# Performance work log

Measured on AMD Instinct MI355X. Metric: run time of the kernel, lower is better.

## Reference

```python
import jax, jax.numpy as jnp
import numpy as np
from jax import lax

K = 7            # pool_size / PSROI_BINS
C_OUT = 10       # output channels per bin (features has K*K*C_OUT channels)
FEAT_STRIDE = 16
LAMDA = 0.1
SAMPLES = 2      # bilinear sample points per bin side
H = W = 200
C_IN = K * K * C_OUT  # 490
N_ROIS = 512


def setup_inputs() -> dict:
    key = jax.random.key(0)
    k1, k2, k3, k4 = jax.random.split(key, 4)
    features = jax.random.normal(k1, (1, H, W, C_IN), jnp.float32)
    conv_w = jax.random.truncated_normal(k2, -2.0, 2.0, (3, 3, C_IN, 2 * K * K), jnp.float32) * 0.01
    img = H * FEAT_STRIDE  # image-space extent
    cxy = jax.random.uniform(k3, (N_ROIS, 2), minval=0.0, maxval=img - 1.0)
    wh = jax.random.uniform(k4, (N_ROIS, 2), minval=64.0, maxval=640.0)
    x1 = jnp.clip(cxy[:, 0] - wh[:, 0] * 0.5, 0.0, img - 2.0)
    y1 = jnp.clip(cxy[:, 1] - wh[:, 1] * 0.5, 0.0, img - 2.0)
    x2 = jnp.clip(x1 + wh[:, 0], x1 + 1.0, img - 1.0)
    y2 = jnp.clip(y1 + wh[:, 1], y1 + 1.0, img - 1.0)
    rois = jnp.stack([jnp.zeros(N_ROIS), x1, y1, x2, y2], axis=-1)  # [N,5]
    return {"features": features, "rois": rois, "conv_w": conv_w}


def _bilinear(feat, y, x):
    """feat [H,W,C]; y,x arbitrary equal shapes -> [..., C]."""
    Hf, Wf = feat.shape[0], feat.shape[1]
    y = jnp.clip(y, 0.0, Hf - 1.0)
    x = jnp.clip(x, 0.0, Wf - 1.0)
    y0 = jnp.floor(y)
    x0 = jnp.floor(x)
    y0i = y0.astype(jnp.int32)
    x0i = x0.astype(jnp.int32)
    y1i = jnp.minimum(y0i + 1, Hf - 1)
    x1i = jnp.minimum(x0i + 1, Wf - 1)
    wy = (y - y0)[..., None]
    wx = (x - x0)[..., None]
    v00 = feat[y0i, x0i]
    v01 = feat[y0i, x1i]
    v10 = feat[y1i, x0i]
    v11 = feat[y1i, x1i]
    return (v00 * (1 - wy) * (1 - wx) + v01 * (1 - wy) * wx
            + v10 * wy * (1 - wx) + v11 * wy * wx)


def _ps_roi(feat, box, cpg, offsets):
    """Position-sensitive RoI avg pooling with optional per-bin offsets.
    feat [H,W,K*K*cpg]; box (x1,y1,x2,y2) image coords; offsets [K,K,2] (dx,dy)
    in image coords or None. Returns [K,K,cpg]."""
    x1, y1, x2, y2 = box
    fx1 = x1 / FEAT_STRIDE
    fy1 = y1 / FEAT_STRIDE
    bw = (x2 - x1 + 1.0) / FEAT_STRIDE / K
    bh = (y2 - y1 + 1.0) / FEAT_STRIDE / K
    idx = jnp.arange(K, dtype=feat.dtype)
    s = (jnp.arange(SAMPLES, dtype=feat.dtype) + 0.5) / SAMPLES
    sx = fx1 + (idx[:, None] + s[None, :]) * bw  # [K(j), S]
    sy = fy1 + (idx[:, None] + s[None, :]) * bh  # [K(i), S]
    gx = jnp.broadcast_to(sx[None, :, None, :], (K, K, SAMPLES, SAMPLES))
    gy = jnp.broadcast_to(sy[:, None, :, None], (K, K, SAMPLES, SAMPLES))
    if offsets is not None:
        off = offsets / FEAT_STRIDE  # image -> feature coords
        gx = gx + off[..., 0][:, :, None, None]
        gy = gy + off[..., 1][:, :, None, None]
    vals = _bilinear(feat, gy, gx)                     # [K,K,S,S,K*K*cpg]
    vals = vals.reshape(K, K, SAMPLES, SAMPLES, K * K, cpg)
    bin_idx = (jnp.arange(K)[:, None] * K + jnp.arange(K)[None, :])  # [K,K]
    sel = jnp.take_along_axis(
        vals, bin_idx[:, :, None, None, None, None], axis=4)[..., 0, :]
    return sel.mean(axis=(2, 3))  # [K,K,cpg]


def reference(features, rois, conv_w):
    # 3x3 same conv producing 2*K*K offset channels (no bias)
    offset_map = lax.conv_general_dilated(
        features, conv_w, (1, 1), 'SAME',
        dimension_numbers=('NHWC', 'HWIO', 'NHWC'))[0]  # [H,W,2*K*K]
    feat0 = features[0]  # [H,W,K*K*C_OUT]

    def one_roi(roi):
        x1, y1, x2, y2 = roi[1], roi[2], roi[3], roi[4]
        rw = x2 - x1 + 1.0
        rh = y2 - y1 + 1.0
        box = (x1, y1, x2, y2)
        # stage 1: pool the offset map position-sensitively -> [K,K,2]
        off = _ps_roi(offset_map, box, 2, None).reshape(-1, 2)
        off = jnp.stack((off[:, 0] * rw * LAMDA,
                         off[:, 1] * rh * LAMDA), axis=-1).reshape(K, K, 2)
        # stage 2: deformable PS-RoI pooling of the features -> [K,K,C_OUT]
        return _ps_roi(feat0, box, C_OUT, off)

    return jax.vmap(one_roi)(rois)  # [N, K, K, C_OUT]
```

## Files before the change

### kernel.cpp

```cpp
#include <hip/hip_runtime.h>
#include <hip/hip_bf16.h>

#define Hh   200
#define Ww   200
#define CIN  490
#define OCN  98
#define KK   7
#define COUT 10
#define NROIS 512
#define PIX  8

#define PH   202
#define PW   202
#define PC   512
#define NPIX (Hh * Ww)
#define KCN  16
#define NF   7
#define NUNITS 144
#define NGRAN  36

typedef __attribute__((ext_vector_type(8))) short short8;
typedef __attribute__((ext_vector_type(4))) float float4v;

__global__ __launch_bounds__(256) void pack_feat_kernel(
    const float* __restrict__ feat, __hip_bfloat16* __restrict__ pf)
{
    int tid = blockIdx.x * 256 + threadIdx.x;
    if (tid >= PH * PW * (PC / 8)) return;
    int c8  = (tid & 63) * 8;
    int pix = tid >> 6;
    int py = pix / PW, px = pix % PW;
    __hip_bfloat16* dst = pf + (size_t)pix * PC + c8;
    bool interior = (py >= 1 && py <= Hh && px >= 1 && px <= Ww);

    __hip_bfloat16 v[8];
    if (interior && c8 + 8 <= CIN) {
        const float* s = feat + ((size_t)(py - 1) * Ww + (px - 1)) * CIN + c8;
#pragma unroll
        for (int q = 0; q < 4; ++q) {
            float2 f2 = *reinterpret_cast<const float2*>(s + q * 2);
            v[q * 2]     = __float2bfloat16(f2.x);
            v[q * 2 + 1] = __float2bfloat16(f2.y);
        }
    } else {
        const float* s = interior ? feat + ((size_t)(py - 1) * Ww + (px - 1)) * CIN : nullptr;
#pragma unroll
        for (int j = 0; j < 8; ++j) {
            float val = (interior && (c8 + j) < CIN) ? s[c8 + j] : 0.f;
            v[j] = __float2bfloat16(val);
        }
    }
    *reinterpret_cast<short8*>(dst) = *reinterpret_cast<short8*>(v);
}

__global__ __launch_bounds__(256) void pack_w_kernel(
    const float* __restrict__ w, __hip_bfloat16* __restrict__ bp)
{
    int idx = blockIdx.x * 256 + threadIdx.x;
    if (idx >= NUNITS * NF * 64 * 8) return;
    int j = idx & 7;
    int l = (idx >> 3) & 63;
    int f = (idx >> 9) % NF;
    int u = idx / (NF * 512);
    int tap = u / KCN, kc = u % KCN;
    int k = kc * 32 + ((l >> 4) * 8) + j;
    int n = f * 16 + (l & 15);
    float val = (k < CIN && n < OCN) ? w[((size_t)tap * CIN + k) * OCN + n] : 0.f;
    bp[idx] = __float2bfloat16(val);
}

__global__ __launch_bounds__(640) void conv_mfma_kernel(
    const short* __restrict__ pf,
    const short* __restrict__ bp,
    float* __restrict__ om)
{
    __shared__ short bsm[8 * 3584];

    int l = threadIdx.x & 63;
    int w = threadIdx.x >> 6;
    int m0 = blockIdx.x * 160 + w * 16;

    int row = m0 + (l & 15);
    int y = row / Ww, x = row % Ww;
    const short* abase = pf + ((size_t)(y * PW + x) * PC) + ((l >> 4) * 8);

    float4v acc[NF];
#pragma unroll
    for (int f = 0; f < NF; ++f) acc[f] = (float4v){0.f, 0.f, 0.f, 0.f};

    auto aAddr = [&](int u) -> const short* {
        int tap = u >> 4, kc = u & 15;
        int ky = tap / 3, kx = tap % 3;
        return abase + (ky * PW + kx) * PC + kc * 32;
    };

    {
#pragma unroll
        for (int s = 0; s < 3; ++s) {
            int i = w + s * 10;
            if (i < 28) {
                int u = i / 7, f = i % 7;
                short8 v = *reinterpret_cast<const short8*>(
                    bp + ((size_t)(u * NF + f)) * 512 + l * 8);
                *reinterpret_cast<short8*>(&bsm[(u & 7) * 3584 + f * 512 + l * 8]) = v;
            }
        }
    }
    short8 a0 = *reinterpret_cast<const short8*>(aAddr(0));
    short8 a1 = *reinterpret_cast<const short8*>(aAddr(1));
    short8 a2 = *reinterpret_cast<const short8*>(aAddr(2));
    short8 a3 = *reinterpret_cast<const short8*>(aAddr(3));
    __syncthreads();

    for (int g = 0; g < NGRAN; ++g) {
        bool more = (g < NGRAN - 1);
        int u0n = (g + 1) * 4;

        short8 st0, st1, st2;
        int off0 = -1, off1 = -1, off2 = -1;
        if (more) {
            {
                int i = w;
                int uu = u0n + i / 7, f = i % 7;
                st0 = *reinterpret_cast<const short8*>(
                    bp + ((size_t)(uu * NF + f)) * 512 + l * 8);
                off0 = (uu & 7) * 3584 + f * 512 + l * 8;
            }
            {
                int i = w + 10;
                int uu = u0n + i / 7, f = i % 7;
                st1 = *reinterpret_cast<const short8*>(
                    bp + ((size_t)(uu * NF + f)) * 512 + l * 8);
                off1 = (uu & 7) * 3584 + f * 512 + l * 8;
            }
            if (w + 20 < 28) {
                int i = w + 20;
                int uu = u0n + i / 7, f = i % 7;
                st2 = *reinterpret_cast<const short8*>(
                    bp + ((size_t)(uu * NF + f)) * 512 + l * 8);
                off2 = (uu & 7) * 3584 + f * 512 + l * 8;
            }
        }
        short8 n0, n1, n2, n3;
        if (more) {
            n0 = *reinterpret_cast<const short8*>(aAddr(u0n + 0));
            n1 = *reinterpret_cast<const short8*>(aAddr(u0n + 1));
            n2 = *reinterpret_cast<const short8*>(aAddr(u0n + 2));
            n3 = *reinterpret_cast<const short8*>(aAddr(u0n + 3));
        }

        int u0 = g * 4;
#define COMPUTE_UNIT(J, AREG)                                                   \
        {                                                                       \
            int sbase = ((u0 + J) & 7) * 3584 + l * 8;                          \
            _Pragma("unroll")                                                   \
            for (int f = 0; f < NF; ++f) {                                      \
                short8 b = *reinterpret_cast<short8*>(&bsm[sbase + f * 512]);   \
                acc[f] = __builtin_amdgcn_mfma_f32_16x16x32_bf16(               \
                    AREG, b, acc[f], 0, 0, 0);                                  \
            }                                                                   \
        }
        COMPUTE_UNIT(0, a0)
        COMPUTE_UNIT(1, a1)
        COMPUTE_UNIT(2, a2)
        COMPUTE_UNIT(3, a3)
#undef COMPUTE_UNIT

        if (off0 >= 0) *reinterpret_cast<short8*>(&bsm[off0]) = st0;
        if (off1 >= 0) *reinterpret_cast<short8*>(&bsm[off1]) = st1;
        if (off2 >= 0) *reinterpret_cast<short8*>(&bsm[off2]) = st2;
        if (more) { a0 = n0; a1 = n1; a2 = n2; a3 = n3; }
        __syncthreads();
    }

    int n = l & 15;
    int rbase = m0 + ((l >> 4) * 4);
#pragma unroll
    for (int f = 0; f < NF; ++f) {
        int col = f * 16 + n;
        if (col < OCN) {
#pragma unroll
            for (int j = 0; j < 4; ++j)
                om[(size_t)(rbase + j) * OCN + col] = acc[f][j];
        }
    }
}

__global__ __launch_bounds__(256) void conv3x3_kernel(
    const float* __restrict__ feat, const float* __restrict__ w,
    const float* __restrict__ zero, float* __restrict__ om)
{
    int idx = blockIdx.x * blockDim.x + threadIdx.x;
    if (idx >= Hh * (Ww / PIX) * OCN) return;
    int oc = idx % OCN;
    int g  = idx / OCN;
    int x0 = (g % (Ww / PIX)) * PIX;
    int y  = g / (Ww / PIX);

    float acc[PIX];
#pragma unroll
    for (int p = 0; p < PIX; ++p) acc[p] = 0.f;

    for (int ky = 0; ky < 3; ++ky) {
        int yy = y + ky - 1;
        if (yy < 0 || yy >= Hh) continue;
        const float* frow = feat + (size_t)yy * Ww * CIN;
        for (int kx = 0; kx < 3; ++kx) {
            const float* wp = w + ((ky * 3 + kx) * CIN) * OCN + oc;
            const float* fp[PIX];
#pragma unroll
            for (int p = 0; p < PIX; ++p) {
                int xx = x0 + p + kx - 1;
                fp[p] = (xx >= 0 && xx < Ww) ? (frow + (size_t)xx * CIN) : zero;
            }
            for (int ic = 0; ic < CIN; ic += 2) {
                float w0 = wp[ic * OCN];
                float w1 = wp[(ic + 1) * OCN];
#pragma unroll
                for (int p = 0; p < PIX; ++p) {
                    float2 f = *reinterpret_cast<const float2*>(fp[p] + ic);
                    acc[p] = fmaf(f.x, w0, acc[p]);
                    acc[p] = fmaf(f.y, w1, acc[p]);
                }
            }
        }
    }
    float* orow = om + ((size_t)y * Ww + x0) * OCN + oc;
#pragma unroll
    for (int p = 0; p < PIX; ++p) orow[p * OCN] = acc[p];
}

__device__ __forceinline__ void bilin_setup(float y, float x,
    int& i00, int& i01, int& i10, int& i11,
    float& w00, float& w01, float& w10, float& w11)
{
    y = fminf(fmaxf(y, 0.f), 199.f);
    x = fminf(fmaxf(x, 0.f), 199.f);
    float y0f = floorf(y), x0f = floorf(x);
    int y0 = (int)y0f, x0i = (int)x0f;
    int y1 = min(y0 + 1, 199), x1 = min(x0i + 1, 199);
    float wy = y - y0f, wx = x - x0f;
    i00 = y0 * Ww + x0i;  i01 = y0 * Ww + x1;
    i10 = y1 * Ww + x0i;  i11 = y1 * Ww + x1;
    w00 = (1.f - wy) * (1.f - wx);
    w01 = (1.f - wy) * wx;
    w10 = wy * (1.f - wx);
    w11 = wy * wx;
}

__global__ __launch_bounds__(256) void psroi_kernel(
    const float* __restrict__ feat, const float* __restrict__ rois,
    const float* __restrict__ om, float* __restrict__ out)
{
    int n = blockIdx.x;
    int t = threadIdx.x;

    float x1 = rois[n * 5 + 1], y1 = rois[n * 5 + 2];
    float x2 = rois[n * 5 + 3], y2 = rois[n * 5 + 4];
    float rw = x2 - x1 + 1.0f, rh = y2 - y1 + 1.0f;
    float fx1 = x1 * 0.0625f, fy1 = y1 * 0.0625f;
    float bw = (rw * 0.0625f) / 7.0f;
    float bh = (rh * 0.0625f) / 7.0f;

    __shared__ float offs[49][2];

    if (t < 49) {
        int bi = t / 7, bj = t % 7;
        float ax = 0.f, ay = 0.f;
#pragma unroll
        for (int ss = 0; ss < 4; ++ss) {
            float sj = ((float)(ss & 1) + 0.5f) * 0.5f;
            float si = ((float)(ss >> 1) + 0.5f) * 0.5f;
            float gx = fx1 + ((float)bj + sj) * bw;
            float gy = fy1 + ((float)bi + si) * bh;
            int i00, i01, i10, i11; float w00, w01, w10, w11;
            bilin_setup(gy, gx, i00, i01, i10, i11, w00, w01, w10, w11);
            int c0 = t * 2;
            const float* p00 = om + (size_t)i00 * OCN + c0;
            const float* p01 = om + (size_t)i01 * OCN + c0;
            const float* p10 = om + (size_t)i10 * OCN + c0;
            const float* p11 = om + (size_t)i11 * OCN + c0;
            ax += w00 * p00[0] + w01 * p01[0] + w10 * p10[0] + w11 * p11[0];
            ay += w00 * p00[1] + w01 * p01[1] + w10 * p10[1] + w11 * p11[1];
        }
        offs[t][0] = ax * 0.25f * rw * 0.1f * 0.0625f;
        offs[t][1] = ay * 0.25f * rh * 0.1f * 0.0625f;
    }
    __syncthreads();

    for (int o = t; o < KK * KK * COUT; o += blockDim.x) {
        int bin = o / COUT, c = o % COUT;
        int bi = bin / 7, bj = bin % 7;
        float dx = offs[bin][0], dy = offs[bin][1];
        int ch = bin * COUT + c;
        float acc = 0.f;
#pragma unroll
        for (int ss = 0; ss < 4; ++ss) {
            float sj = ((float)(ss & 1) + 0.5f) * 0.5f;
            float si = ((float)(ss >> 1) + 0.5f) * 0.5f;
            float gx = fx1 + ((float)bj + sj) * bw + dx;
            float gy = fy1 + ((float)bi + si) * bh + dy;
            int i00, i01, i10, i11; float w00, w01, w10, w11;
            bilin_setup(gy, gx, i00, i01, i10, i11, w00, w01, w10, w11);
            acc += w00 * feat[(size_t)i00 * CIN + ch]
                 + w01 * feat[(size_t)i01 * CIN + ch]
                 + w10 * feat[(size_t)i10 * CIN + ch]
                 + w11 * feat[(size_t)i11 * CIN + ch];
        }
        out[(size_t)n * (KK * KK * COUT) + o] = acc * 0.25f;
    }
}

extern "C" void kernel_launch(void* const* d_in, const int* in_sizes, int n_in,
                              void* d_out, int out_size, void* d_ws, size_t ws_size,
                              hipStream_t stream) {
    const float* feat = (const float*)d_in[0];
    const float* rois = (const float*)d_in[1];
    const float* w    = (const float*)d_in[2];
    float* out = (float*)d_out;

    const size_t OM_BYTES = (size_t)NPIX * OCN * 4;
    const size_t BP_BYTES = (size_t)NUNITS * NF * 64 * 8 * 2;
    const size_t PF_BYTES = (size_t)PH * PW * PC * 2;
    const size_t NEEDED = OM_BYTES + BP_BYTES + PF_BYTES;

    if (ws_size >= NEEDED) {
        float* om = (float*)d_ws;
        __hip_bfloat16* bp = (__hip_bfloat16*)((char*)d_ws + OM_BYTES);
        __hip_bfloat16* pf = (__hip_bfloat16*)((char*)d_ws + OM_BYTES + BP_BYTES);

        int wThreads = NUNITS * NF * 64 * 8;
        pack_w_kernel<<<(wThreads + 255) / 256, 256, 0, stream>>>(w, bp);
        int fThreads = PH * PW * (PC / 8);
        pack_feat_kernel<<<(fThreads + 255) / 256, 256, 0, stream>>>(feat, pf);
        conv_mfma_kernel<<<250, 640, 0, stream>>>(
            (const short*)pf, (const short*)bp, om);
        psroi_kernel<<<NROIS, 256, 0, stream>>>(feat, rois, om, out);
    } else {
        float* zero = (float*)d_ws;
        float* om   = (float*)d_ws + 1024;
        hipMemsetAsync(d_ws, 0, 4096, stream);
        int convThreads = Hh * (Ww / PIX) * OCN;
        conv3x3_kernel<<<(convThreads + 255) / 256, 256, 0, stream>>>(feat, w, zero, om);
        psroi_kernel<<<NROIS, 256, 0, stream>>>(feat, rois, om, out);
    }
}
```

Baseline: 96.75 us.

## Fuse feature bf16 packing into conv MFMA kernel and vectorize psroi gather

Removes the separate pack_feat kernel that converted and padded the features to bf16, and makes the conv MFMA kernel read the fp32 features directly. Padding is handled with per-tap boundary masks, and the tail of the channel range with a guarded partial load. The reduction order changes to kc-major/tap-minor, with pack_w updated to match, and the conv kernel gets a two-blocks-per-SM launch bound. The psroi stage-2 loop now has each thread handle two channels with float2 loads and stores. This saves a full write and reread of the padded bf16 feature buffer and one launch, but the conv loads double in bytes and need in-loop conversion and branching.

```diff
diff --git a/kernel.cpp b/kernel.cpp
--- a/kernel.cpp
+++ b/kernel.cpp
@@ -10,9 +10,6 @@
 #define NROIS 512
 #define PIX  8
 
-#define PH   202
-#define PW   202
-#define PC   512
 #define NPIX (Hh * Ww)
 #define KCN  16
 #define NF   7
@@ -21,37 +18,6 @@
 
 typedef __attribute__((ext_vector_type(8))) short short8;
 typedef __attribute__((ext_vector_type(4))) float float4v;
-
-__global__ __launch_bounds__(256) void pack_feat_kernel(
-    const float* __restrict__ feat, __hip_bfloat16* __restrict__ pf)
-{
-    int tid = blockIdx.x * 256 + threadIdx.x;
-    if (tid >= PH * PW * (PC / 8)) return;
-    int c8  = (tid & 63) * 8;
-    int pix = tid >> 6;
-    int py = pix / PW, px = pix % PW;
-    __hip_bfloat16* dst = pf + (size_t)pix * PC + c8;
-    bool interior = (py >= 1 && py <= Hh && px >= 1 && px <= Ww);
-
-    __hip_bfloat16 v[8];
-    if (interior && c8 + 8 <= CIN) {
-        const float* s = feat + ((size_t)(py - 1) * Ww + (px - 1)) * CIN + c8;
-#pragma unroll
-        for (int q = 0; q < 4; ++q) {
-            float2 f2 = *reinterpret_cast<const float2*>(s + q * 2);
-            v[q * 2]     = __float2bfloat16(f2.x);
-            v[q * 2 + 1] = __float2bfloat16(f2.y);
-        }
-    } else {
-        const float* s = interior ? feat + ((size_t)(py - 1) * Ww + (px - 1)) * CIN : nullptr;
-#pragma unroll
-        for (int j = 0; j < 8; ++j) {
-            float val = (interior && (c8 + j) < CIN) ? s[c8 + j] : 0.f;
-            v[j] = __float2bfloat16(val);
-        }
-    }
-    *reinterpret_cast<short8*>(dst) = *reinterpret_cast<short8*>(v);
-}
 
 __global__ __launch_bounds__(256) void pack_w_kernel(
     const float* __restrict__ w, __hip_bfloat16* __restrict__ bp)
@@ -62,15 +28,15 @@
     int l = (idx >> 3) & 63;
     int f = (idx >> 9) % NF;
     int u = idx / (NF * 512);
-    int tap = u / KCN, kc = u % KCN;
+    int kc = u / 9, tap = u % 9;
     int k = kc * 32 + ((l >> 4) * 8) + j;
     int n = f * 16 + (l & 15);
     float val = (k < CIN && n < OCN) ? w[((size_t)tap * CIN + k) * OCN + n] : 0.f;
     bp[idx] = __float2bfloat16(val);
 }
 
-__global__ __launch_bounds__(640) void conv_mfma_kernel(
-    const short* __restrict__ pf,
+__global__ __launch_bounds__(640, 2) void conv_mfma_kernel(
+    const float* __restrict__ feat,
     const short* __restrict__ bp,
     float* __restrict__ om)
 {
@@ -82,39 +48,91 @@
 
     int row = m0 + (l & 15);
     int y = row / Ww, x = row % Ww;
-    const short* abase = pf + ((size_t)(y * PW + x) * PC) + ((l >> 4) * 8);
+    int grp4 = l >> 4;
+    int grpOff = grp4 * 8;
+    int pixBase = (y * Ww + x) * CIN;
+
+    int smask = 0;
+#pragma unroll
+    for (int tp = 0; tp < 9; ++tp) {
+        int yy = y + tp / 3 - 1, xx = x + tp % 3 - 1;
+        if (yy >= 0 && yy < Hh && xx >= 0 && xx < Ww) smask |= (1 << tp);
+    }
 
     float4v acc[NF];
 #pragma unroll
     for (int f = 0; f < NF; ++f) acc[f] = (float4v){0.f, 0.f, 0.f, 0.f};
 
-    auto aAddr = [&](int u) -> const short* {
-        int tap = u >> 4, kc = u & 15;
-        int ky = tap / 3, kx = tap % 3;
-        return abase + (ky * PW + kx) * PC + kc * 32;
-    };
-
-    {
-#pragma unroll
-        for (int s = 0; s < 3; ++s) {
-            int i = w + s * 10;
-            if (i < 28) {
-                int u = i / 7, f = i % 7;
-                short8 v = *reinterpret_cast<const short8*>(
-                    bp + ((size_t)(u * NF + f)) * 512 + l * 8);
-                *reinterpret_cast<short8*>(&bsm[(u & 7) * 3584 + f * 512 + l * 8]) = v;
-            }
-        }
-    }
-    short8 a0 = *reinterpret_cast<const short8*>(aAddr(0));
-    short8 a1 = *reinterpret_cast<const short8*>(aAddr(1));
-    short8 a2 = *reinterpret_cast<const short8*>(aAddr(2));
-    short8 a3 = *reinterpret_cast<const short8*>(aAddr(3));
+    float2 preq[4][4];
+    short8 c0, c1, c2, c3;
+
+#define LOAD_A(J, UEXPR)                                                        \
+    {                                                                           \
+        int u_ = (UEXPR);                                                       \
+        int kc_ = u_ / 9, tap_ = u_ - kc_ * 9;                                  \
+        int toff_ = ((tap_ / 3 - 1) * Ww + (tap_ % 3 - 1)) * CIN;               \
+        bool v_ = (smask >> tap_) & 1;                                          \
+        const float* p_ = feat + (pixBase + toff_ + kc_ * 32 + grpOff);         \
+        float2 z_ = {0.f, 0.f};                                                 \
+        preq[J][0] = z_; preq[J][1] = z_; preq[J][2] = z_; preq[J][3] = z_;     \
+        if (kc_ < 15) {                                                         \
+            if (v_) {                                                           \
+                preq[J][0] = *reinterpret_cast<const float2*>(p_);              \
+                preq[J][1] = *reinterpret_cast<const float2*>(p_ + 2);          \
+                preq[J][2] = *reinterpret_cast<const float2*>(p_ + 4);          \
+                preq[J][3] = *reinterpret_cast<const float2*>(p_ + 6);          \
+            }                                                                   \
+        } else {                                                                \
+            if (v_ && grp4 == 0) {                                              \
+                preq[J][0] = *reinterpret_cast<const float2*>(p_);              \
+                preq[J][1] = *reinterpret_cast<const float2*>(p_ + 2);          \
+                preq[J][2] = *reinterpret_cast<const float2*>(p_ + 4);          \
+                preq[J][3] = *reinterpret_cast<const float2*>(p_ + 6);          \
+            } else if (v_ && grp4 == 1) {                                       \
+                preq[J][0] = *reinterpret_cast<const float2*>(p_);   \
+            }                                                                   \
+        }                                                                       \
+    }
+
+#define CVT_A(J, DST)                                                           \
+    {                                                                           \
+        short8 s_;                                                              \
+        __hip_bfloat16 h_;                                                      \
+        h_ = __float2bfloat16(preq[J][0].x); s_[0] = *reinterpret_cast<short*>(&h_); \
+        h_ = __float2bfloat16(preq[J][0].y); s_[1] = *reinterpret_cast<short*>(&h_); \
+        h_ = __float2bfloat16(preq[J][1].x); s_[2] = *reinterpret_cast<short*>(&h_); \
+        h_ = __float2bfloat16(preq[J][1].y); s_[3] = *reinterpret_cast<short*>(&h_); \
+        h_ = __float2bfloat16(preq[J][2].x); s_[4] = *reinterpret_cast<short*>(&h_); \
+        h_ = __float2bfloat16(preq[J][2].y); s_[5] = *reinterpret_cast<short*>(&h_); \
+        h_ = __float2bfloat16(preq[J][3].x); s_[6] = *reinterpret_cast<short*>(&h_); \
+        h_ = __float2bfloat16(preq[J][3].y); s_[7] = *reinterpret_cast<short*>(&h_); \
+        DST = s_;                                                               \
+    }
+
+#pragma unroll
+    for (int s = 0; s < 3; ++s) {
+        int i = w + s * 10;
+        if (i < 28) {
+            int u = i / 7, f = i % 7;
+            short8 v = *reinterpret_cast<const short8*>(
+                bp + ((size_t)(u * NF + f)) * 512 + l * 8);
+            *reinterpret_cast<short8*>(&bsm[(u & 7) * 3584 + f * 512 + l * 8]) = v;
+        }
+    }
+    LOAD_A(0, 0)
+    LOAD_A(1, 1)
+    LOAD_A(2, 2)
+    LOAD_A(3, 3)
     __syncthreads();
 
     for (int g = 0; g < NGRAN; ++g) {
         bool more = (g < NGRAN - 1);
         int u0n = (g + 1) * 4;
+
+        CVT_A(0, c0)
+        CVT_A(1, c1)
+        CVT_A(2, c2)
+        CVT_A(3, c3)
 
         short8 st0, st1, st2;
         int off0 = -1, off1 = -1, off2 = -1;
@@ -141,12 +159,11 @@
                 off2 = (uu & 7) * 3584 + f * 512 + l * 8;
             }
         }
-        short8 n0, n1, n2, n3;
         if (more) {
-            n0 = *reinterpret_cast<const short8*>(aAddr(u0n + 0));
-            n1 = *reinterpret_cast<const short8*>(aAddr(u0n + 1));
-            n2 = *reinterpret_cast<const short8*>(aAddr(u0n + 2));
-            n3 = *reinterpret_cast<const short8*>(aAddr(u0n + 3));
+            LOAD_A(0, u0n + 0)
+            LOAD_A(1, u0n + 1)
+            LOAD_A(2, u0n + 2)
+            LOAD_A(3, u0n + 3)
         }
 
         int u0 = g * 4;
@@ -160,18 +177,19 @@
                     AREG, b, acc[f], 0, 0, 0);                                  \
             }                                                                   \
         }
-        COMPUTE_UNIT(0, a0)
-        COMPUTE_UNIT(1, a1)
-        COMPUTE_UNIT(2, a2)
-        COMPUTE_UNIT(3, a3)
+        COMPUTE_UNIT(0, c0)
+        COMPUTE_UNIT(1, c1)
+        COMPUTE_UNIT(2, c2)
+        COMPUTE_UNIT(3, c3)
 #undef COMPUTE_UNIT
 
         if (off0 >= 0) *reinterpret_cast<short8*>(&bsm[off0]) = st0;
         if (off1 >= 0) *reinterpret_cast<short8*>(&bsm[off1]) = st1;
         if (off2 >= 0) *reinterpret_cast<short8*>(&bsm[off2]) = st2;
-        if (more) { a0 = n0; a1 = n1; a2 = n2; a3 = n3; }
         __syncthreads();
     }
+#undef LOAD_A
+#undef CVT_A
 
     int n = l & 15;
     int rbase = m0 + ((l >> 4) * 4);
@@ -288,12 +306,12 @@
     }
     __syncthreads();
 
-    for (int o = t; o < KK * KK * COUT; o += blockDim.x) {
-        int bin = o / COUT, c = o % COUT;
+    if (t < 245) {
+        int bin = t / 5, cp = t % 5;
         int bi = bin / 7, bj = bin % 7;
         float dx = offs[bin][0], dy = offs[bin][1];
-        int ch = bin * COUT + c;
-        float acc = 0.f;
+        int ch0 = bin * COUT + cp * 2;
+        float accx = 0.f, accy = 0.f;
 #pragma unroll
         for (int ss = 0; ss < 4; ++ss) {
             float sj = ((float)(ss & 1) + 0.5f) * 0.5f;
@@ -302,12 +320,16 @@
             float gy = fy1 + ((float)bi + si) * bh + dy;
             int i00, i01, i10, i11; float w00, w01, w10, w11;
             bilin_setup(gy, gx, i00, i01, i10, i11, w00, w01, w10, w11);
-            acc += w00 * feat[(size_t)i00 * CIN + ch]
-                 + w01 * feat[(size_t)i01 * CIN + ch]
-                 + w10 * feat[(size_t)i10 * CIN + ch]
-                 + w11 * feat[(size_t)i11 * CIN + ch];
-        }
-        out[(size_t)n * (KK * KK * COUT) + o] = acc * 0.25f;
+            float2 v00 = *reinterpret_cast<const float2*>(feat + (size_t)i00 * CIN + ch0);
+            float2 v01 = *reinterpret_cast<const float2*>(feat + (size_t)i01 * CIN + ch0);
+            float2 v10 = *reinterpret_cast<const float2*>(feat + (size_t)i10 * CIN + ch0);
+            float2 v11 = *reinterpret_cast<const float2*>(feat + (size_t)i11 * CIN + ch0);
+            accx += w00 * v00.x + w01 * v01.x + w10 * v10.x + w11 * v11.x;
+            accy += w00 * v00.y + w01 * v01.y + w10 * v10.y + w11 * v11.y;
+        }
+        float2 res = {accx * 0.25f, accy * 0.25f};
+        *reinterpret_cast<float2*>(
+            out + (size_t)n * (KK * KK * COUT) + bin * COUT + cp * 2) = res;
     }
 }
 
@@ -321,20 +343,15 @@
 
     const size_t OM_BYTES = (size_t)NPIX * OCN * 4;
     const size_t BP_BYTES = (size_t)NUNITS * NF * 64 * 8 * 2;
-    const size_t PF_BYTES = (size_t)PH * PW * PC * 2;
-    const size_t NEEDED = OM_BYTES + BP_BYTES + PF_BYTES;
+    const size_t NEEDED = OM_BYTES + BP_BYTES;
 
     if (ws_size >= NEEDED) {
         float* om = (float*)d_ws;
         __hip_bfloat16* bp = (__hip_bfloat16*)((char*)d_ws + OM_BYTES);
-        __hip_bfloat16* pf = (__hip_bfloat16*)((char*)d_ws + OM_BYTES + BP_BYTES);
 
         int wThreads = NUNITS * NF * 64 * 8;
         pack_w_kernel<<<(wThreads + 255) / 256, 256, 0, stream>>>(w, bp);
-        int fThreads = PH * PW * (PC / 8);
-        pack_feat_kernel<<<(fThreads + 255) / 256, 256, 0, stream>>>(feat, pf);
-        conv_mfma_kernel<<<250, 640, 0, stream>>>(
-            (const short*)pf, (const short*)bp, om);
+        conv_mfma_kernel<<<250, 640, 0, stream>>>(feat, (const short*)bp, om);
         psroi_kernel<<<NROIS, 256, 0, stream>>>(feat, rois, om, out);
     } else {
         float* zero = (float*)d_ws;
```

New measurement: 133.2 us. 1.38x slower.
